# Performance work log

Hardware: AMD Instinct MI355X
Metric: run time of the kernel (lower is better)

Reference implementation:

```python
import jax, jax.numpy as jnp
import numpy as np

N, D = 8192, 1024
Q = 4096
DK = 512
DV = 256


def setup_inputs() -> dict:
    key = jax.random.key(0)
    k1, k2, k3, k4, k5, k6 = jax.random.split(key, 6)
    return {
        "search_x": jax.random.normal(k1, (N, D), dtype=jnp.float32),
        "search_y": jax.random.normal(k2, (N, DV), dtype=jnp.float32),
        "query_x": jax.random.normal(k3, (Q, D), dtype=jnp.float32),
        "mask": jax.random.randint(k4, (Q, N), 0, 2, dtype=jnp.int64),
        "Wk": jax.random.normal(k5, (D, DK), dtype=jnp.float32) / np.sqrt(D),
        "Wq": jax.random.normal(k6, (D, DK), dtype=jnp.float32) / np.sqrt(D),
    }


def reference(search_x, search_y, query_x, mask, Wk, Wq):
    # key/query modules: bias-free linear projections (n_keys == 1 after _ensure_key_shape)
    keys = search_x @ Wk            # [N, DK]
    qk = query_x @ Wq               # [Q, DK]
    scale = 1.0 / jnp.sqrt(jnp.asarray(DK, dtype=keys.dtype))
    logits = (qk @ keys.T) * scale  # [Q, N]  (== broadcast mul+sum in original)
    # masked softmax over the search dimension (dim=1)
    m = mask > 0                    # [Q, N]
    neg = jnp.finfo(logits.dtype).min
    p = jax.nn.softmax(jnp.where(m, logits, neg), axis=1)
    p = jnp.where(m, p, 0.0)
    # values = noop_value_module(search_x, search_y) = search_y  [N, DV]
    res = p @ search_y              # [Q, DV]
    return res[:, None, :]          # [Q, n_keys=1, DV], matching original output shape
```

## Files before the change

kernel.cpp:

```cpp
#include <hip/hip_runtime.h>
#include <hip/hip_fp16.h>

typedef _Float16 half4v __attribute__((ext_vector_type(4)));
typedef _Float16 half8v __attribute__((ext_vector_type(8)));
typedef float floatx4 __attribute__((ext_vector_type(4)));

#define GLOBAL_AS __attribute__((address_space(1)))
#define LDS_AS __attribute__((address_space(3)))

__device__ __forceinline__ void async_copy16(const _Float16* g, _Float16* l) {
    __builtin_amdgcn_global_load_lds((const GLOBAL_AS unsigned int*)g,
                                     (LDS_AS unsigned int*)l, 16, 0, 0);
}

__global__ __launch_bounds__(256) void k_f32_to_f16(const float* __restrict__ in,
                                                    _Float16* __restrict__ out, int n) {
    int i = (blockIdx.x * 256 + threadIdx.x) * 4;
    if (i >= n) return;
    float4 v = *(const float4*)(in + i);
    half4v h;
    h[0] = (_Float16)v.x; h[1] = (_Float16)v.y; h[2] = (_Float16)v.z; h[3] = (_Float16)v.w;
    *(half4v*)(out + i) = h;
}

__global__ __launch_bounds__(256) void k_transpose_f16(const float* __restrict__ in,
                                                       _Float16* __restrict__ out,
                                                       int R, int C) {
    __shared__ float tile[32][33];
    int bc = blockIdx.x * 32;
    int br = blockIdx.y * 32;
    int tx = threadIdx.x & 31, ty = threadIdx.x >> 5;
#pragma unroll
    for (int i = 0; i < 32; i += 8)
        tile[ty + i][tx] = in[(size_t)(br + ty + i) * C + bc + tx];
    __syncthreads();
#pragma unroll
    for (int i = 0; i < 32; i += 8)
        out[(size_t)(bc + ty + i) * R + br + tx] = (_Float16)tile[tx][ty + i];
}

template <int OUT_MODE>
__global__ __launch_bounds__(256) void k_gemm_nt(const _Float16* __restrict__ A,
                                                 const _Float16* __restrict__ B,
                                                 void* __restrict__ C,
                                                 int M, int N, int K, int kChunk,
                                                 float scale) {
    __shared__ __align__(16) _Float16 As[128 * 64];
    __shared__ __align__(16) _Float16 Bs[128 * 64];
    const int tid  = threadIdx.x;
    const int lane = tid & 63;
    const int wave = tid >> 6;
    const int wm   = (wave >> 1) * 64;
    const int wn   = (wave & 1) * 64;
    const int quad = lane >> 4;
    const int lr   = lane & 15;
    const long m0 = (long)blockIdx.y * 128;
    const long n0 = (long)blockIdx.x * 128;
    const int kBegin = blockIdx.z * kChunk;
    const int kEnd   = kBegin + kChunk;

    floatx4 acc[4][4] = {};

    const int rl = lane >> 3;
    const int gc = (lane & 7) ^ rl;
    const long arow = m0 + wave * 32 + rl;
    const long brow = n0 + wave * 32 + rl;

    for (int kt = kBegin; kt < kEnd; kt += 64) {
        const _Float16* Ap = A + arow * (long)K + kt + gc * 8;
        const _Float16* Bp = B + brow * (long)K + kt + gc * 8;
        _Float16* Al = &As[(wave * 32) * 64];
        _Float16* Bl = &Bs[(wave * 32) * 64];
#pragma unroll
        for (int i = 0; i < 4; ++i) {
            async_copy16(Ap + (long)(i * 8) * K, Al + i * 8 * 64);
            async_copy16(Bp + (long)(i * 8) * K, Bl + i * 8 * 64);
        }
        __syncthreads();

#pragma unroll
        for (int kk = 0; kk < 64; kk += 32) {
            half8v af[4], bf[4];
            const int cg = (kk >> 3) + quad;
            const int sl = (cg ^ (lr & 7)) * 8;
#pragma unroll
            for (int i = 0; i < 4; ++i)
                af[i] = *(const half8v*)&As[(wm + i * 16 + lr) * 64 + sl];
#pragma unroll
            for (int j = 0; j < 4; ++j)
                bf[j] = *(const half8v*)&Bs[(wn + j * 16 + lr) * 64 + sl];
#pragma unroll
            for (int i = 0; i < 4; ++i)
#pragma unroll
                for (int j = 0; j < 4; ++j)
                    acc[i][j] = __builtin_amdgcn_mfma_f32_16x16x32_f16(af[i], bf[j], acc[i][j], 0, 0, 0);
        }
        __syncthreads();
    }

#pragma unroll
    for (int i = 0; i < 4; ++i) {
        long rbase = m0 + wm + i * 16 + quad * 4;
#pragma unroll
        for (int j = 0; j < 4; ++j) {
            long col = n0 + wn + j * 16 + lr;
#pragma unroll
            for (int r = 0; r < 4; ++r) {
                float val = acc[i][j][r] * scale;
                if (OUT_MODE == 0)
                    ((_Float16*)C)[(rbase + r) * (long)N + col] = (_Float16)val;
                else
                    ((float*)C)[(size_t)blockIdx.z * M * N + (rbase + r) * (long)N + col] = val;
            }
        }
    }
}

__global__ __launch_bounds__(256) void k_reduce8(const float* __restrict__ part,
                                                 float* __restrict__ out, int n) {
    int i = (blockIdx.x * 256 + threadIdx.x) * 4;
    if (i >= n) return;
    float4 s = *(const float4*)(part + i);
#pragma unroll
    for (int z = 1; z < 8; ++z) {
        float4 v = *(const float4*)(part + (size_t)z * n + i);
        s.x += v.x; s.y += v.y; s.z += v.z; s.w += v.w;
    }
    *(float4*)(out + i) = s;
}

__global__ __launch_bounds__(256) void k_softmax(_Float16* __restrict__ logits,
                                                 const int* __restrict__ mask) {
    const int q   = blockIdx.x;
    const int tid = threadIdx.x;
    _Float16* row   = logits + (size_t)q * 8192;
    const int* mrow = mask + (size_t)q * 8192;

    float v[32];
    unsigned mb = 0;
    float lmax = -3.0e38f;
#pragma unroll
    for (int i = 0; i < 8; ++i) {
        int base = i * 1024 + tid * 4;
        int4 mm  = *(const int4*)(mrow + base);
        half4v h = *(const half4v*)(row + base);
#pragma unroll
        for (int j = 0; j < 4; ++j) v[i * 4 + j] = (float)h[j];
        if (mm.x > 0) { mb |= 1u << (i * 4 + 0); lmax = fmaxf(lmax, v[i * 4 + 0]); }
        if (mm.y > 0) { mb |= 1u << (i * 4 + 1); lmax = fmaxf(lmax, v[i * 4 + 1]); }
        if (mm.z > 0) { mb |= 1u << (i * 4 + 2); lmax = fmaxf(lmax, v[i * 4 + 2]); }
        if (mm.w > 0) { mb |= 1u << (i * 4 + 3); lmax = fmaxf(lmax, v[i * 4 + 3]); }
    }
#pragma unroll
    for (int off = 32; off > 0; off >>= 1) lmax = fmaxf(lmax, __shfl_xor(lmax, off, 64));
    __shared__ float redmax[4], redsum[4];
    if ((tid & 63) == 0) redmax[tid >> 6] = lmax;
    __syncthreads();
    lmax = fmaxf(fmaxf(redmax[0], redmax[1]), fmaxf(redmax[2], redmax[3]));

    float lsum = 0.f;
#pragma unroll
    for (int i = 0; i < 32; ++i) {
        float e = ((mb >> i) & 1u) ? __expf(v[i] - lmax) : 0.f;
        v[i] = e;
        lsum += e;
    }
#pragma unroll
    for (int off = 32; off > 0; off >>= 1) lsum += __shfl_xor(lsum, off, 64);
    if ((tid & 63) == 0) redsum[tid >> 6] = lsum;
    __syncthreads();
    lsum = redsum[0] + redsum[1] + redsum[2] + redsum[3];
    float inv = lsum > 0.f ? 1.f / lsum : 0.f;

#pragma unroll
    for (int i = 0; i < 8; ++i) {
        int base = i * 1024 + tid * 4;
        half4v h;
#pragma unroll
        for (int j = 0; j < 4; ++j) h[j] = (_Float16)(v[i * 4 + j] * inv);
        *(half4v*)(row + base) = h;
    }
}

extern "C" void kernel_launch(void* const* d_in, const int* in_sizes, int n_in,
                              void* d_out, int out_size, void* d_ws, size_t ws_size,
                              hipStream_t stream) {
    const float* search_x = (const float*)d_in[0];
    const float* search_y = (const float*)d_in[1];
    const float* query_x  = (const float*)d_in[2];
    const int*   mask     = (const int*)d_in[3];
    const float* Wk       = (const float*)d_in[4];
    const float* Wq       = (const float*)d_in[5];
    (void)in_sizes; (void)n_in; (void)ws_size; (void)out_size;

    char* p = (char*)d_ws;
    _Float16* xh   = (_Float16*)p; p += (size_t)8192 * 1024 * 2;
    _Float16* qh   = (_Float16*)p; p += (size_t)4096 * 1024 * 2;
    _Float16* wkT  = (_Float16*)p; p += (size_t)512 * 1024 * 2;
    _Float16* wqT  = (_Float16*)p; p += (size_t)512 * 1024 * 2;
    _Float16* yT   = (_Float16*)p; p += (size_t)256 * 8192 * 2;
    _Float16* keys = (_Float16*)p; p += (size_t)8192 * 512 * 2;
    _Float16* qk   = (_Float16*)p; p += (size_t)4096 * 512 * 2;
    _Float16* lg   = (_Float16*)p; p += (size_t)4096 * 8192 * 2;
    float*    part = (float*)p;    p += (size_t)8 * 4096 * 256 * 4;

    k_f32_to_f16<<<8192, 256, 0, stream>>>(search_x, xh, 8192 * 1024);
    k_f32_to_f16<<<4096, 256, 0, stream>>>(query_x, qh, 4096 * 1024);
    k_transpose_f16<<<dim3(16, 32), 256, 0, stream>>>(Wk, wkT, 1024, 512);
    k_transpose_f16<<<dim3(16, 32), 256, 0, stream>>>(Wq, wqT, 1024, 512);
    k_transpose_f16<<<dim3(8, 256), 256, 0, stream>>>(search_y, yT, 8192, 256);

    k_gemm_nt<0><<<dim3(4, 64, 1), 256, 0, stream>>>(xh, wkT, keys, 8192, 512, 1024, 1024, 1.0f);
    k_gemm_nt<0><<<dim3(4, 32, 1), 256, 0, stream>>>(qh, wqT, qk, 4096, 512, 1024, 1024, 1.0f);
    k_gemm_nt<0><<<dim3(64, 32, 1), 256, 0, stream>>>(qk, keys, lg, 4096, 8192, 512, 512,
                                                      0.04419417382415922f);
    k_softmax<<<4096, 256, 0, stream>>>(lg, mask);
    k_gemm_nt<1><<<dim3(2, 32, 8), 256, 0, stream>>>(lg, yT, part, 4096, 256, 8192, 1024, 1.0f);
    k_reduce8<<<1024, 256, 0, stream>>>(part, (float*)d_out, 4096 * 256);
}
```

Before: 370.1 us.

## Merge conversions, remap GEMM blocks per XCD, and replace split-K reduce with atomics

The two f32-to-f16 conversion launches become a single launch. GEMM workgroup IDs are remapped so neighbouring tiles are scheduled together on each of the 8 chiplets, which should improve L2 reuse. The final split-K GEMM now accumulates straight into the zeroed output with float atomics, using 4 K-splits instead of 8, so the partial buffer and reduce kernel are gone. Atomics make the summation order nondeterministic and add an extra zeroing launch.

```diff
diff --git a/kernel.cpp b/kernel.cpp
--- a/kernel.cpp
+++ b/kernel.cpp
@@ -13,14 +13,24 @@
                                      (LDS_AS unsigned int*)l, 16, 0, 0);
 }
 
-__global__ __launch_bounds__(256) void k_f32_to_f16(const float* __restrict__ in,
-                                                    _Float16* __restrict__ out, int n) {
+__global__ __launch_bounds__(256) void k_f32_to_f16_2(const float* __restrict__ a,
+                                                      _Float16* __restrict__ oa, int na,
+                                                      const float* __restrict__ b,
+                                                      _Float16* __restrict__ ob, int nb) {
     int i = (blockIdx.x * 256 + threadIdx.x) * 4;
-    if (i >= n) return;
-    float4 v = *(const float4*)(in + i);
+    const float* src;
+    _Float16* dst;
+    if (i < na) {
+        src = a + i; dst = oa + i;
+    } else {
+        int j = i - na;
+        if (j >= nb) return;
+        src = b + j; dst = ob + j;
+    }
+    float4 v = *(const float4*)src;
     half4v h;
     h[0] = (_Float16)v.x; h[1] = (_Float16)v.y; h[2] = (_Float16)v.z; h[3] = (_Float16)v.w;
-    *(half4v*)(out + i) = h;
+    *(half4v*)dst = h;
 }
 
 __global__ __launch_bounds__(256) void k_transpose_f16(const float* __restrict__ in,
@@ -37,6 +47,12 @@
 #pragma unroll
     for (int i = 0; i < 32; i += 8)
         out[(size_t)(bc + ty + i) * R + br + tx] = (_Float16)tile[tx][ty + i];
+}
+
+__global__ __launch_bounds__(256) void k_zero_f32(float* __restrict__ p, int n) {
+    int i = (blockIdx.x * 256 + threadIdx.x) * 4;
+    if (i >= n) return;
+    *(float4*)(p + i) = make_float4(0.f, 0.f, 0.f, 0.f);
 }
 
 template <int OUT_MODE>
@@ -54,8 +70,16 @@
     const int wn   = (wave & 1) * 64;
     const int quad = lane >> 4;
     const int lr   = lane & 15;
-    const long m0 = (long)blockIdx.y * 128;
-    const long n0 = (long)blockIdx.x * 128;
+
+    const int nx  = gridDim.x;
+    const int nwg = nx * gridDim.y;
+    int id = blockIdx.y * nx + blockIdx.x;
+    id = (id & 7) * (nwg >> 3) + (id >> 3);
+    const int bx = id % nx;
+    const int by = id / nx;
+
+    const long m0 = (long)by * 128;
+    const long n0 = (long)bx * 128;
     const int kBegin = blockIdx.z * kChunk;
     const int kEnd   = kBegin + kChunk;
 
@@ -107,26 +131,16 @@
 #pragma unroll
             for (int r = 0; r < 4; ++r) {
                 float val = acc[i][j][r] * scale;
-                if (OUT_MODE == 0)
+                if (OUT_MODE == 0) {
                     ((_Float16*)C)[(rbase + r) * (long)N + col] = (_Float16)val;
-                else
-                    ((float*)C)[(size_t)blockIdx.z * M * N + (rbase + r) * (long)N + col] = val;
+                } else {
+                    __hip_atomic_fetch_add(&((float*)C)[(rbase + r) * (long)N + col],
+                                           val, __ATOMIC_RELAXED,
+                                           __HIP_MEMORY_SCOPE_AGENT);
+                }
             }
         }
     }
-}
-
-__global__ __launch_bounds__(256) void k_reduce8(const float* __restrict__ part,
-                                                 float* __restrict__ out, int n) {
-    int i = (blockIdx.x * 256 + threadIdx.x) * 4;
-    if (i >= n) return;
-    float4 s = *(const float4*)(part + i);
-#pragma unroll
-    for (int z = 1; z < 8; ++z) {
-        float4 v = *(const float4*)(part + (size_t)z * n + i);
-        s.x += v.x; s.y += v.y; s.z += v.z; s.w += v.w;
-    }
-    *(float4*)(out + i) = s;
 }
 
 __global__ __launch_bounds__(256) void k_softmax(_Float16* __restrict__ logits,
@@ -202,19 +216,19 @@
     _Float16* keys = (_Float16*)p; p += (size_t)8192 * 512 * 2;
     _Float16* qk   = (_Float16*)p; p += (size_t)4096 * 512 * 2;
     _Float16* lg   = (_Float16*)p; p += (size_t)4096 * 8192 * 2;
-    float*    part = (float*)p;    p += (size_t)8 * 4096 * 256 * 4;
-
-    k_f32_to_f16<<<8192, 256, 0, stream>>>(search_x, xh, 8192 * 1024);
-    k_f32_to_f16<<<4096, 256, 0, stream>>>(query_x, qh, 4096 * 1024);
+
+    k_f32_to_f16_2<<<12288, 256, 0, stream>>>(search_x, xh, 8192 * 1024,
+                                              query_x, qh, 4096 * 1024);
     k_transpose_f16<<<dim3(16, 32), 256, 0, stream>>>(Wk, wkT, 1024, 512);
     k_transpose_f16<<<dim3(16, 32), 256, 0, stream>>>(Wq, wqT, 1024, 512);
     k_transpose_f16<<<dim3(8, 256), 256, 0, stream>>>(search_y, yT, 8192, 256);
+    k_zero_f32<<<1024, 256, 0, stream>>>((float*)d_out, 4096 * 256);
 
     k_gemm_nt<0><<<dim3(4, 64, 1), 256, 0, stream>>>(xh, wkT, keys, 8192, 512, 1024, 1024, 1.0f);
     k_gemm_nt<0><<<dim3(4, 32, 1), 256, 0, stream>>>(qh, wqT, qk, 4096, 512, 1024, 1024, 1.0f);
     k_gemm_nt<0><<<dim3(64, 32, 1), 256, 0, stream>>>(qk, keys, lg, 4096, 8192, 512, 512,
                                                       0.04419417382415922f);
     k_softmax<<<4096, 256, 0, stream>>>(lg, mask);
-    k_gemm_nt<1><<<dim3(2, 32, 8), 256, 0, stream>>>(lg, yT, part, 4096, 256, 8192, 1024, 1.0f);
-    k_reduce8<<<1024, 256, 0, stream>>>(part, (float*)d_out, 4096 * 256);
-}
+    k_gemm_nt<1><<<dim3(2, 32, 4), 256, 0, stream>>>(lg, yT, (float*)d_out,
+                                                     4096, 256, 8192, 2048, 1.0f);
+}
```

Result: slower. 392.1 us (+6.0%).
